# Optimization experiments

Hardware: AMD Instinct MI355X
Metric: run time of the kernel (lower is better)

## Reference

```python
import jax, jax.numpy as jnp
import numpy as np
import math

B, N, D, H = 16, 1024, 1024, 8
HD = D // H
SCALE = 1.0 / math.sqrt(D // 8)
NEG = -1e30


def setup_inputs() -> dict:
    key = jax.random.key(0)
    ks = jax.random.split(key, 10)
    s = 0.02
    return {
        "x": jax.random.normal(ks[0], (B, N, D), dtype=jnp.float32),
        "x_mask": jax.random.randint(ks[1], (B, N), 0, 2, dtype=jnp.int32),
        "Wq": jax.random.normal(ks[2], (H, D, HD), dtype=jnp.float32) * s,
        "bq": jnp.zeros((H, HD), dtype=jnp.float32),
        "Wk": jax.random.normal(ks[3], (H, D, HD), dtype=jnp.float32) * s,
        "bk": jnp.zeros((H, HD), dtype=jnp.float32),
        "Wv": jax.random.normal(ks[4], (H, D, HD), dtype=jnp.float32) * s,
        "bv": jnp.zeros((H, HD), dtype=jnp.float32),
        "Wfc": jax.random.normal(ks[5], (D, D), dtype=jnp.float32) * s,
        "bfc": jnp.zeros((D,), dtype=jnp.float32),
    }


def reference(x, x_mask, Wq, bq, Wk, bk, Wv, bv, Wfc, bfc):
    # per-head projections, stacked: [B, H, N, HD]
    q = jnp.einsum("bnd,hde->bhne", x, Wq) + bq[None, :, None, :]
    k = jnp.einsum("bnd,hde->bhne", x, Wk) + bk[None, :, None, :]
    v = jnp.einsum("bnd,hde->bhne", x, Wv) + bv[None, :, None, :]
    # pairwise padding mask: mask & mask^T  ->  outer product for 0/1 values
    m = x_mask.astype(x.dtype)  # [B, N]
    mask = m[:, :, None] * m[:, None, :]  # [B, N, N]
    scores = jnp.einsum("bhne,bhme->bhnm", q, k) * SCALE  # [B, H, N, N]
    scores = scores * mask[:, None] + NEG * (1.0 - mask[:, None])
    attn = jax.nn.softmax(scores, axis=-1)
    o = jnp.einsum("bhnm,bhme->bhne", attn, v)  # [B, H, N, HD]
    # concat heads along feature dim (head order preserved)
    o = jnp.transpose(o, (0, 2, 1, 3)).reshape(B, N, D)
    out = o @ Wfc + bfc  # final fc; F.dropout result is discarded in source
    return out
```

## Files before the change

kernel.cpp:

```cpp
#include <hip/hip_runtime.h>
#include <hip/hip_bf16.h>
#include <math.h>

#define BN 1024
#define DD 1024
#define NB 16
#define NH 8
#define HDIM 128

typedef __attribute__((ext_vector_type(8))) short bf16x8;
typedef __attribute__((ext_vector_type(4))) float f32x4;
typedef __attribute__((ext_vector_type(4))) unsigned short ushort4v;

#define DEV __device__ __forceinline__

DEV unsigned short f2bf(float f) {
  unsigned u = __float_as_uint(f);
  u = (u + 0x7fffu + ((u >> 16) & 1u)) >> 16;
  return (unsigned short)u;
}

DEV f32x4 mfma16(bf16x8 a, bf16x8 b, f32x4 c) {
  return __builtin_amdgcn_mfma_f32_16x16x32_bf16(a, b, c, 0, 0, 0);
}

DEV void async16(const unsigned short* g, unsigned short* l) {
  __builtin_amdgcn_global_load_lds(
      (const __attribute__((address_space(1))) unsigned short*)g,
      (__attribute__((address_space(3))) unsigned short*)l, 16, 0, 0);
}

__global__ __launch_bounds__(256) void prep_kernel(
    const float* __restrict__ x, const float* __restrict__ Wq,
    const float* __restrict__ Wk, const float* __restrict__ Wv,
    const float* __restrict__ Wfc, unsigned short* __restrict__ x_bf,
    unsigned short* __restrict__ wqkvT, unsigned short* __restrict__ wfcT) {
  __shared__ float tile[32][33];
  const int bx = blockIdx.x, tid = threadIdx.x;
  if (bx < 16384) {
    int i = bx * 256 + tid;
    const float4* p = (const float4*)x;
    float4 v = p[i];
    ushort4v o;
    o[0] = f2bf(v.x); o[1] = f2bf(v.y); o[2] = f2bf(v.z); o[3] = f2bf(v.w);
    *(ushort4v*)(x_bf + (size_t)i * 4) = o;
    return;
  }
  const int tx = tid & 31, ty = tid >> 5;
  if (bx < 19456) {
    int idx = bx - 16384;
    int k0 = (idx & 31) * 32, e0 = ((idx >> 5) & 3) * 32, z = idx >> 7;
    int which = z >> 3, h = z & 7;
    const float* in = (which == 0 ? Wq : (which == 1 ? Wk : Wv)) + (size_t)h * DD * HDIM;
#pragma unroll
    for (int i = 0; i < 4; ++i)
      tile[ty + i * 8][tx] = in[(size_t)(k0 + ty + i * 8) * HDIM + e0 + tx];
    __syncthreads();
    int rowbase = which * 1024 + h * 128 + e0;
#pragma unroll
    for (int i = 0; i < 4; ++i)
      wqkvT[(size_t)(rowbase + ty + i * 8) * DD + k0 + tx] = f2bf(tile[tx][ty + i * 8]);
  } else {
    int idx = bx - 19456;
    int d0 = (idx & 31) * 32, c0 = (idx >> 5) * 32;
#pragma unroll
    for (int i = 0; i < 4; ++i)
      tile[ty + i * 8][tx] = Wfc[(size_t)(d0 + ty + i * 8) * DD + c0 + tx];
    __syncthreads();
#pragma unroll
    for (int i = 0; i < 4; ++i)
      wfcT[(size_t)(c0 + ty + i * 8) * DD + d0 + tx] = f2bf(tile[tx][ty + i * 8]);
  }
}

template <int MODE>
__global__ __launch_bounds__(512, 2) void gemm256_kernel(
    const unsigned short* __restrict__ A, const unsigned short* __restrict__ Bt,
    const float* __restrict__ bias0, const float* __restrict__ bias1,
    const float* __restrict__ bias2, unsigned short* __restrict__ out0,
    unsigned short* __restrict__ out1, unsigned short* __restrict__ out2,
    float* __restrict__ outf) {
  __shared__ unsigned short As[2][256 * 64];
  __shared__ unsigned short Bs[2][256 * 64];
  const int tid = threadIdx.x;
  const int w = tid >> 6, lane = tid & 63, quad = lane >> 4, l15 = lane & 15;
  const int wr = w >> 2, wc = w & 3;

  constexpr int NBN = (MODE == 0) ? 12 : 4;
  constexpr int CPX = (MODE == 0) ? 96 : 32;
  const int bid = blockIdx.x;
  const int swz = (bid & 7) * CPX + (bid >> 3);
  const int mblk = swz / NBN, nblk = swz - mblk * NBN;
  const int m0 = mblk << 8, n0 = nblk << 8;

  const int srow = tid >> 3;
  const int gch = ((tid & 7) - srow) & 7;
  const unsigned short* ag = A + (size_t)(m0 + srow) * 1024 + gch * 8;
  const unsigned short* bg = Bt + (size_t)(n0 + srow) * 1024 + gch * 8;
  const int wbase = w * 512;

  const int sl0 = ((quad + l15) & 7) * 8;
  const int sl1 = ((quad + l15 + 4) & 7) * 8;

  f32x4 acc[8][4] = {};
  bf16x8 af[4][2];
  bf16x8 bfr[4][2];

#define STAGE_A_LO(buf, kb) do { \
    async16(ag + (kb), &As[buf][0] + wbase); \
    async16(ag + (kb) + 64 * 1024, &As[buf][64 * 64] + wbase); } while (0)
#define STAGE_A_HI(buf, kb) do { \
    async16(ag + (kb) + 128 * 1024, &As[buf][128 * 64] + wbase); \
    async16(ag + (kb) + 192 * 1024, &As[buf][192 * 64] + wbase); } while (0)
#define STAGE_B_LO(buf, kb) do { \
    async16(bg + (kb), &Bs[buf][0] + wbase); \
    async16(bg + (kb) + 64 * 1024, &Bs[buf][64 * 64] + wbase); } while (0)
#define STAGE_B_HI(buf, kb) do { \
    async16(bg + (kb) + 128 * 1024, &Bs[buf][128 * 64] + wbase); \
    async16(bg + (kb) + 192 * 1024, &Bs[buf][192 * 64] + wbase); } while (0)

  STAGE_A_LO(0, 0); STAGE_B_LO(0, 0); STAGE_B_HI(0, 0); STAGE_A_HI(0, 0);
  STAGE_A_LO(1, 64); STAGE_B_LO(1, 64); STAGE_B_HI(1, 64); STAGE_A_HI(1, 64);
  asm volatile("s_waitcnt vmcnt(8)" ::: "memory");
  __builtin_amdgcn_s_barrier();

  for (int t = 0; t < 16; ++t) {
    const int cur = t & 1;
    const unsigned short* ac = &As[cur][0];
    const unsigned short* bc = &Bs[cur][0];
    const int kb2 = ((t + 2) & 15) * 64;

#pragma unroll
    for (int mt = 0; mt < 4; ++mt) {
      const unsigned short* rp = ac + (wr * 16 + mt * 32 + l15) * 64;
      af[mt][0] = *(const bf16x8*)(rp + sl0);
      af[mt][1] = *(const bf16x8*)(rp + sl1);
    }
#pragma unroll
    for (int nt = 0; nt < 2; ++nt) {
      const unsigned short* rp = bc + (wc * 16 + nt * 64 + l15) * 64;
      bfr[nt][0] = *(const bf16x8*)(rp + sl0);
      bfr[nt][1] = *(const bf16x8*)(rp + sl1);
    }
    __builtin_amdgcn_s_barrier();
    asm volatile("s_waitcnt lgkmcnt(0)" ::: "memory");
    __builtin_amdgcn_s_setprio(1);
#pragma unroll
    for (int mt = 0; mt < 4; ++mt)
#pragma unroll
      for (int nt = 0; nt < 2; ++nt) {
        acc[mt][nt] = mfma16(af[mt][0], bfr[nt][0], acc[mt][nt]);
        acc[mt][nt] = mfma16(af[mt][1], bfr[nt][1], acc[mt][nt]);
      }
    __builtin_amdgcn_s_setprio(0);
    __builtin_amdgcn_s_barrier();

#pragma unroll
    for (int nt = 0; nt < 2; ++nt) {
      const unsigned short* rp = bc + (wc * 16 + 128 + nt * 64 + l15) * 64;
      bfr[2 + nt][0] = *(const bf16x8*)(rp + sl0);
      bfr[2 + nt][1] = *(const bf16x8*)(rp + sl1);
    }
    STAGE_A_LO(cur, kb2);
    __builtin_amdgcn_s_barrier();
    asm volatile("s_waitcnt lgkmcnt(0)" ::: "memory");
    __builtin_amdgcn_s_setprio(1);
#pragma unroll
    for (int mt = 0; mt < 4; ++mt)
#pragma unroll
      for (int nt = 0; nt < 2; ++nt) {
        acc[mt][2 + nt] = mfma16(af[mt][0], bfr[2 + nt][0], acc[mt][2 + nt]);
        acc[mt][2 + nt] = mfma16(af[mt][1], bfr[2 + nt][1], acc[mt][2 + nt]);
      }
    __builtin_amdgcn_s_setprio(0);
    __builtin_amdgcn_s_barrier();

#pragma unroll
    for (int mt = 0; mt < 4; ++mt) {
      const unsigned short* rp = ac + (wr * 16 + 128 + mt * 32 + l15) * 64;
      af[mt][0] = *(const bf16x8*)(rp + sl0);
      af[mt][1] = *(const bf16x8*)(rp + sl1);
    }
    STAGE_B_LO(cur, kb2);
    __builtin_amdgcn_s_barrier();
    asm volatile("s_waitcnt lgkmcnt(0)" ::: "memory");
    __builtin_amdgcn_s_setprio(1);
#pragma unroll
    for (int mt = 0; mt < 4; ++mt)
#pragma unroll
      for (int nt = 0; nt < 2; ++nt) {
        acc[4 + mt][2 + nt] = mfma16(af[mt][0], bfr[2 + nt][0], acc[4 + mt][2 + nt]);
        acc[4 + mt][2 + nt] = mfma16(af[mt][1], bfr[2 + nt][1], acc[4 + mt][2 + nt]);
      }
    __builtin_amdgcn_s_setprio(0);
    __builtin_amdgcn_s_barrier();

    STAGE_B_HI(cur, kb2);
    STAGE_A_HI(cur, kb2);
    asm volatile("s_waitcnt vmcnt(8)" ::: "memory");
    __builtin_amdgcn_s_barrier();
    __builtin_amdgcn_s_setprio(1);
#pragma unroll
    for (int mt = 0; mt < 4; ++mt)
#pragma unroll
      for (int nt = 0; nt < 2; ++nt) {
        acc[4 + mt][nt] = mfma16(af[mt][0], bfr[nt][0], acc[4 + mt][nt]);
        acc[4 + mt][nt] = mfma16(af[mt][1], bfr[nt][1], acc[4 + mt][nt]);
      }
    __builtin_amdgcn_s_setprio(0);
    __builtin_amdgcn_s_barrier();
  }
#undef STAGE_A_LO
#undef STAGE_A_HI
#undef STAGE_B_LO
#undef STAGE_B_HI

  if constexpr (MODE == 0) {
    const int seg = n0 >> 10;
    const float* bp = (seg == 0) ? bias0 : (seg == 1 ? bias1 : bias2);
#pragma unroll
    for (int ai = 0; ai < 8; ++ai) {
      int mb = m0 + wr * 16 + ai * 32 + quad * 4;
      int bb = mb >> 10, nn = mb & 1023;
#pragma unroll
      for (int nt = 0; nt < 4; ++nt) {
        int c = n0 + wc * 16 + nt * 64 + l15;
        int cc = c & 1023;
        int h = cc >> 7, e = cc & 127;
        float bias = bp[cc];
        if (seg == 2) {
          ushort4v pv;
#pragma unroll
          for (int r = 0; r < 4; ++r) pv[r] = f2bf(acc[ai][nt][r] + bias);
          *(ushort4v*)(out2 + ((size_t)(bb * NH + h) * HDIM + e) * BN + nn) = pv;
        } else {
          unsigned short* op = (seg == 0) ? out0 : out1;
#pragma unroll
          for (int r = 0; r < 4; ++r)
            op[(((size_t)bb * NH + h) * BN + (nn + r)) * HDIM + e] =
                f2bf(acc[ai][nt][r] + bias);
        }
      }
    }
  } else {
#pragma unroll
    for (int ai = 0; ai < 8; ++ai) {
      int mb = m0 + wr * 16 + ai * 32 + quad * 4;
#pragma unroll
      for (int nt = 0; nt < 4; ++nt) {
        int c = n0 + wc * 16 + nt * 64 + l15;
        float bias = bias0[c];
#pragma unroll
        for (int r = 0; r < 4; ++r)
          outf[(size_t)(mb + r) * DD + c] = acc[ai][nt][r] + bias;
      }
    }
  }
}

__global__ __launch_bounds__(256, 2) void flash_attn_kernel(
    const unsigned short* __restrict__ Q, const unsigned short* __restrict__ Kk,
    const unsigned short* __restrict__ Vt, const int* __restrict__ xmask,
    unsigned short* __restrict__ O) {
  __shared__ unsigned short k_s[64 * 128];
  __shared__ unsigned short v_s[2][128 * 64];
  __shared__ unsigned short p_s[128 * 72];
  __shared__ float l_s[2][128];

  const float CL2E = 0.08838834764831845f * 1.44269504088896f;

  const int tid = threadIdx.x;
  const int w = tid >> 6, lane = tid & 63, quad = lane >> 4, l15 = lane & 15;
  const int wq = w >> 1, wk = w & 1;
  const int lin = blockIdx.x;
  const int bh = lin & 127, qb = lin >> 7;
  const int b = bh >> 3, h = bh & 7;
  const int q0 = qb * 128;
  const unsigned short* qp = Q + ((size_t)bh * BN + q0) * HDIM;
  const unsigned short* kp = Kk + (size_t)bh * BN * HDIM;
  const unsigned short* vp = Vt + (size_t)bh * HDIM * BN;
  const int* xm_b = xmask + b * BN;

  bf16x8 qf[4][4];
#pragma unroll
  for (int mt = 0; mt < 4; ++mt)
#pragma unroll
    for (int ks = 0; ks < 4; ++ks)
      qf[mt][ks] = *(const bf16x8*)(qp + (wq * 64 + mt * 16 + l15) * HDIM + ks * 32 + quad * 8);

  int rowm_bits = 0;
#pragma unroll
  for (int mt = 0; mt < 4; ++mt)
#pragma unroll
    for (int r = 0; r < 4; ++r)
      rowm_bits |= (xm_b[q0 + wq * 64 + mt * 16 + quad * 4 + r] ? 1 : 0) << (mt * 4 + r);

  const int krow = lane >> 4;
  const int vrow = lane >> 3;
  const int vch = ((lane & 7) - vrow) & 7;

  float l_lane[4][4] = {};
  f32x4 o_acc[4][4] = {};

#pragma unroll
  for (int i = 0; i < 4; ++i) {
    int rmod = i * 4 + krow;
    int g = ((lane & 15) - rmod) & 15;
    async16(kp + (size_t)(w * 16 + rmod) * HDIM + g * 8, k_s + (w * 16 + i * 4) * 128);
    int e = w * 32 + i * 8 + vrow;
    async16(vp + (size_t)e * BN + vch * 8, v_s[0] + (w * 32 + i * 8) * 64);
  }

  for (int it = 0; it < 16; ++it) {
    const int kb = it * 64;
    int cm0 = xm_b[kb + wk * 32 + l15];
    int cm1 = xm_b[kb + wk * 32 + 16 + l15];
    __syncthreads();

    f32x4 s[4][2] = {};
#pragma unroll
    for (int ks = 0; ks < 4; ++ks) {
      const int sl = ((ks * 4 + quad + l15) & 15) * 8;
      bf16x8 b0 = *(const bf16x8*)(k_s + (wk * 32 + l15) * 128 + sl);
      bf16x8 b1 = *(const bf16x8*)(k_s + (wk * 32 + 16 + l15) * 128 + sl);
#pragma unroll
      for (int mt = 0; mt < 4; ++mt) {
        s[mt][0] = mfma16(qf[mt][ks], b0, s[mt][0]);
        s[mt][1] = mfma16(qf[mt][ks], b1, s[mt][1]);
      }
    }

#pragma unroll
    for (int mt = 0; mt < 4; ++mt)
#pragma unroll
      for (int nt = 0; nt < 2; ++nt) {
        int cmv = nt ? cm1 : cm0;
#pragma unroll
        for (int r = 0; r < 4; ++r) {
          float xs = s[mt][nt][r] * CL2E;
          float t = cmv ? xs : -60.0f;
          int rb = (rowm_bits >> (mt * 4 + r)) & 1;
          float e2 = rb ? t : 0.0f;
          float p = __builtin_amdgcn_exp2f(e2);
          l_lane[mt][r] += p;
          p_s[(wq * 64 + mt * 16 + quad * 4 + r) * 72 + wk * 32 + nt * 16 + l15] = f2bf(p);
        }
      }

    __syncthreads();

    {
      const int kn = (kb + 64) & (BN - 1);
      unsigned short* vb_next = v_s[(it + 1) & 1];
#pragma unroll
      for (int i = 0; i < 4; ++i) {
        int rmod = i * 4 + krow;
        int g = ((lane & 15) - rmod) & 15;
        async16(kp + (size_t)(kn + w * 16 + rmod) * HDIM + g * 8,
                k_s + (w * 16 + i * 4) * 128);
        int e = w * 32 + i * 8 + vrow;
        async16(vp + (size_t)e * BN + kn + vch * 8, vb_next + (w * 32 + i * 8) * 64);
      }
    }

    const unsigned short* vb = v_s[it & 1];
#pragma unroll
    for (int ks2 = 0; ks2 < 2; ++ks2) {
      const int sl = ((ks2 * 4 + quad + l15) & 7) * 8;
      bf16x8 pa[4];
#pragma unroll
      for (int mt = 0; mt < 4; ++mt)
        pa[mt] = *(const bf16x8*)(p_s + (wq * 64 + mt * 16 + l15) * 72 + ks2 * 32 + quad * 8);
#pragma unroll
      for (int et = 0; et < 4; ++et) {
        bf16x8 bv = *(const bf16x8*)(vb + (wk * 64 + et * 16 + l15) * 64 + sl);
#pragma unroll
        for (int mt = 0; mt < 4; ++mt)
          o_acc[mt][et] = mfma16(pa[mt], bv, o_acc[mt][et]);
      }
    }
  }

#pragma unroll
  for (int mt = 0; mt < 4; ++mt)
#pragma unroll
    for (int r = 0; r < 4; ++r) {
      float l = l_lane[mt][r];
#pragma unroll
      for (int off = 1; off < 16; off <<= 1) l += __shfl_xor(l, off, 64);
      if (l15 == 0) l_s[wk][wq * 64 + mt * 16 + quad * 4 + r] = l;
    }
  __syncthreads();

#pragma unroll
  for (int mt = 0; mt < 4; ++mt)
#pragma unroll
    for (int r = 0; r < 4; ++r) {
      int rl = wq * 64 + mt * 16 + quad * 4 + r;
      float inv = 1.0f / (l_s[0][rl] + l_s[1][rl]);
      int row = q0 + rl;
#pragma unroll
      for (int et = 0; et < 4; ++et) {
        int col = h * HDIM + wk * 64 + et * 16 + l15;
        O[((size_t)b * BN + row) * DD + col] = f2bf(o_acc[mt][et][r] * inv);
      }
    }
}

extern "C" void kernel_launch(void* const* d_in, const int* in_sizes, int n_in,
                              void* d_out, int out_size, void* d_ws, size_t ws_size,
                              hipStream_t stream) {
  const float* x = (const float*)d_in[0];
  const int* xmask = (const int*)d_in[1];
  const float* Wq = (const float*)d_in[2];
  const float* bq = (const float*)d_in[3];
  const float* Wk = (const float*)d_in[4];
  const float* bk = (const float*)d_in[5];
  const float* Wv = (const float*)d_in[6];
  const float* bv = (const float*)d_in[7];
  const float* Wfc = (const float*)d_in[8];
  const float* bfc = (const float*)d_in[9];
  float* out = (float*)d_out;

  char* ws = (char*)d_ws;
  unsigned short* x_bf  = (unsigned short*)(ws);
  unsigned short* wqkvT = (unsigned short*)(ws + 33554432);
  unsigned short* wfcT  = (unsigned short*)(ws + 39845888);
  unsigned short* q_bf  = (unsigned short*)(ws + 41943040);
  unsigned short* k_bf  = (unsigned short*)(ws + 75497472);
  unsigned short* vT_bf = (unsigned short*)(ws + 109051904);
  unsigned short* o_bf  = (unsigned short*)(ws + 142606336);

  prep_kernel<<<dim3(20480), dim3(256), 0, stream>>>(x, Wq, Wk, Wv, Wfc, x_bf, wqkvT, wfcT);

  gemm256_kernel<0><<<dim3(768), dim3(512), 0, stream>>>(
      x_bf, wqkvT, bq, bk, bv, q_bf, k_bf, vT_bf, nullptr);

  flash_attn_kernel<<<dim3(1024), dim3(256), 0, stream>>>(q_bf, k_bf, vT_bf, xmask, o_bf);

  gemm256_kernel<1><<<dim3(256), dim3(512), 0, stream>>>(
      o_bf, wfcT, bfc, nullptr, nullptr, nullptr, nullptr, nullptr, out);
}
```

Before: 407.5 us.

## Restructure GEMM main loop into register double-buffered K-half MFMA clusters

Reorganizes the 256x256 GEMM inner loop so LDS fragments are split by K-half (sl0/sl1) and double-buffered in registers: while one 4x4 MFMA cluster runs, the next K-half fragments are read from LDS. The A-high staging for the next tile is moved earlier into the other buffer, reducing barriers per iteration from eight to four and removing the explicit lgkmcnt waits before each cluster. The intent is to overlap LDS reads and global async copies with MFMA issue. It risks hazards from the reordered staging and buffer reuse, and holding both fragment sets raises register pressure.

```diff
diff --git a/kernel.cpp b/kernel.cpp
--- a/kernel.cpp
+++ b/kernel.cpp
@@ -100,11 +100,11 @@
   const int wbase = w * 512;
 
   const int sl0 = ((quad + l15) & 7) * 8;
-  const int sl1 = ((quad + l15 + 4) & 7) * 8;
+  const int sl1 = ((quad + 4 + l15) & 7) * 8;
 
   f32x4 acc[8][4] = {};
-  bf16x8 af[4][2];
-  bf16x8 bfr[4][2];
+  bf16x8 aK0[4], aK1[4];
+  bf16x8 bK0[4], bK1[4];
 
 #define STAGE_A_LO(buf, kb) do { \
     async16(ag + (kb), &As[buf][0] + wbase); \
@@ -118,102 +118,75 @@
 #define STAGE_B_HI(buf, kb) do { \
     async16(bg + (kb) + 128 * 1024, &Bs[buf][128 * 64] + wbase); \
     async16(bg + (kb) + 192 * 1024, &Bs[buf][192 * 64] + wbase); } while (0)
-
-  STAGE_A_LO(0, 0); STAGE_B_LO(0, 0); STAGE_B_HI(0, 0); STAGE_A_HI(0, 0);
-  STAGE_A_LO(1, 64); STAGE_B_LO(1, 64); STAGE_B_HI(1, 64); STAGE_A_HI(1, 64);
+#define READ_A(dst, buf, moff, slx) do { \
+    _Pragma("unroll") \
+    for (int mt = 0; mt < 4; ++mt) \
+      dst[mt] = *(const bf16x8*)(&As[buf][0] + (wr * 16 + (moff) + mt * 32 + l15) * 64 + (slx)); \
+    } while (0)
+#define READ_B(dst, buf, slx) do { \
+    _Pragma("unroll") \
+    for (int nt = 0; nt < 4; ++nt) \
+      dst[nt] = *(const bf16x8*)(&Bs[buf][0] + (wc * 16 + nt * 64 + l15) * 64 + (slx)); \
+    } while (0)
+#define CLUSTER(base, a, b) do { \
+    __builtin_amdgcn_s_setprio(1); \
+    _Pragma("unroll") \
+    for (int mt = 0; mt < 4; ++mt) \
+      _Pragma("unroll") \
+      for (int nt = 0; nt < 4; ++nt) \
+        acc[(base) + mt][nt] = mfma16(a[mt], b[nt], acc[(base) + mt][nt]); \
+    __builtin_amdgcn_s_setprio(0); } while (0)
+
+  STAGE_A_LO(0, 0); STAGE_B_LO(0, 0);
+  STAGE_B_HI(0, 0);
+  STAGE_A_HI(0, 0);
+  STAGE_A_LO(1, 64); STAGE_B_LO(1, 64);
+  STAGE_B_HI(1, 64);
   asm volatile("s_waitcnt vmcnt(8)" ::: "memory");
   __builtin_amdgcn_s_barrier();
+  __builtin_amdgcn_sched_barrier(0);
+  READ_A(aK0, 0, 0, sl0);
+  READ_B(bK0, 0, sl0);
 
   for (int t = 0; t < 16; ++t) {
-    const int cur = t & 1;
-    const unsigned short* ac = &As[cur][0];
-    const unsigned short* bc = &Bs[cur][0];
+    const int cur = t & 1, oth = cur ^ 1;
+    const int kb1 = ((t + 1) & 15) * 64;
     const int kb2 = ((t + 2) & 15) * 64;
 
-#pragma unroll
-    for (int mt = 0; mt < 4; ++mt) {
-      const unsigned short* rp = ac + (wr * 16 + mt * 32 + l15) * 64;
-      af[mt][0] = *(const bf16x8*)(rp + sl0);
-      af[mt][1] = *(const bf16x8*)(rp + sl1);
-    }
-#pragma unroll
-    for (int nt = 0; nt < 2; ++nt) {
-      const unsigned short* rp = bc + (wc * 16 + nt * 64 + l15) * 64;
-      bfr[nt][0] = *(const bf16x8*)(rp + sl0);
-      bfr[nt][1] = *(const bf16x8*)(rp + sl1);
-    }
-    __builtin_amdgcn_s_barrier();
-    asm volatile("s_waitcnt lgkmcnt(0)" ::: "memory");
-    __builtin_amdgcn_s_setprio(1);
-#pragma unroll
-    for (int mt = 0; mt < 4; ++mt)
-#pragma unroll
-      for (int nt = 0; nt < 2; ++nt) {
-        acc[mt][nt] = mfma16(af[mt][0], bfr[nt][0], acc[mt][nt]);
-        acc[mt][nt] = mfma16(af[mt][1], bfr[nt][1], acc[mt][nt]);
-      }
-    __builtin_amdgcn_s_setprio(0);
-    __builtin_amdgcn_s_barrier();
-
-#pragma unroll
-    for (int nt = 0; nt < 2; ++nt) {
-      const unsigned short* rp = bc + (wc * 16 + 128 + nt * 64 + l15) * 64;
-      bfr[2 + nt][0] = *(const bf16x8*)(rp + sl0);
-      bfr[2 + nt][1] = *(const bf16x8*)(rp + sl1);
-    }
-    STAGE_A_LO(cur, kb2);
-    __builtin_amdgcn_s_barrier();
-    asm volatile("s_waitcnt lgkmcnt(0)" ::: "memory");
-    __builtin_amdgcn_s_setprio(1);
-#pragma unroll
-    for (int mt = 0; mt < 4; ++mt)
-#pragma unroll
-      for (int nt = 0; nt < 2; ++nt) {
-        acc[mt][2 + nt] = mfma16(af[mt][0], bfr[2 + nt][0], acc[mt][2 + nt]);
-        acc[mt][2 + nt] = mfma16(af[mt][1], bfr[2 + nt][1], acc[mt][2 + nt]);
-      }
-    __builtin_amdgcn_s_setprio(0);
-    __builtin_amdgcn_s_barrier();
-
-#pragma unroll
-    for (int mt = 0; mt < 4; ++mt) {
-      const unsigned short* rp = ac + (wr * 16 + 128 + mt * 32 + l15) * 64;
-      af[mt][0] = *(const bf16x8*)(rp + sl0);
-      af[mt][1] = *(const bf16x8*)(rp + sl1);
-    }
-    STAGE_B_LO(cur, kb2);
-    __builtin_amdgcn_s_barrier();
-    asm volatile("s_waitcnt lgkmcnt(0)" ::: "memory");
-    __builtin_amdgcn_s_setprio(1);
-#pragma unroll
-    for (int mt = 0; mt < 4; ++mt)
-#pragma unroll
-      for (int nt = 0; nt < 2; ++nt) {
-        acc[4 + mt][2 + nt] = mfma16(af[mt][0], bfr[2 + nt][0], acc[4 + mt][2 + nt]);
-        acc[4 + mt][2 + nt] = mfma16(af[mt][1], bfr[2 + nt][1], acc[4 + mt][2 + nt]);
-      }
-    __builtin_amdgcn_s_setprio(0);
-    __builtin_amdgcn_s_barrier();
-
-    STAGE_B_HI(cur, kb2);
-    STAGE_A_HI(cur, kb2);
+    READ_A(aK1, cur, 0, sl1);
+    READ_B(bK1, cur, sl1);
+    STAGE_A_HI(oth, kb1);
+    CLUSTER(0, aK0, bK0);
+
     asm volatile("s_waitcnt vmcnt(8)" ::: "memory");
     __builtin_amdgcn_s_barrier();
-    __builtin_amdgcn_s_setprio(1);
-#pragma unroll
-    for (int mt = 0; mt < 4; ++mt)
-#pragma unroll
-      for (int nt = 0; nt < 2; ++nt) {
-        acc[4 + mt][nt] = mfma16(af[mt][0], bfr[nt][0], acc[4 + mt][nt]);
-        acc[4 + mt][nt] = mfma16(af[mt][1], bfr[nt][1], acc[4 + mt][nt]);
-      }
-    __builtin_amdgcn_s_setprio(0);
+    __builtin_amdgcn_sched_barrier(0);
+    READ_A(aK0, cur, 128, sl0);
+    CLUSTER(0, aK1, bK1);
     __builtin_amdgcn_s_barrier();
-  }
+
+    STAGE_A_LO(cur, kb2); STAGE_B_LO(cur, kb2);
+    READ_A(aK1, cur, 128, sl1);
+    CLUSTER(4, aK0, bK0);
+
+    STAGE_B_HI(cur, kb2);
+    asm volatile("s_waitcnt vmcnt(8)" ::: "memory");
+    __builtin_amdgcn_s_barrier();
+    __builtin_amdgcn_sched_barrier(0);
+    READ_A(aK0, oth, 0, sl0);
+    READ_B(bK0, oth, sl0);
+    CLUSTER(4, aK1, bK1);
+    __builtin_amdgcn_s_barrier();
+  }
+  asm volatile("s_waitcnt vmcnt(0)" ::: "memory");
+
 #undef STAGE_A_LO
 #undef STAGE_A_HI
 #undef STAGE_B_LO
 #undef STAGE_B_HI
+#undef READ_A
+#undef READ_B
+#undef CLUSTER
 
   if constexpr (MODE == 0) {
     const int seg = n0 >> 10;
```

After: 400.9 us. No clear change (-1.6%).
